# Kernel tuning notes

Hardware: AMD Instinct MI355X
Metric: run time of the kernel (lower is better)

## Reference

```python
import jax, jax.numpy as jnp
import numpy as np

D_MODEL = 1024
N_HEADS = 16
D_HEAD = D_MODEL // N_HEADS
D_FF = 4096
B, S = 4, 1024
EPS = 1e-12


def layer_norm(x, gamma, beta):
    # Faithful to the torch module: unbiased std (ddof=1) and division by (std + eps).
    mean = jnp.mean(x, axis=-1, keepdims=True)
    var = jnp.sum((x - mean) ** 2, axis=-1, keepdims=True) / (x.shape[-1] - 1)
    std = jnp.sqrt(var)
    return gamma * (x - mean) / (std + EPS) + beta


def setup_inputs() -> dict:
    key = jax.random.key(0)
    ks = jax.random.split(key, 10)
    sc = lambda fan_in: 1.0 / np.sqrt(fan_in)
    inp = {
        "x": jax.random.normal(ks[0], (B, S, D_MODEL), dtype=jnp.float32),
        "ln1_g": jnp.ones((D_MODEL,), jnp.float32),
        "ln1_b": jnp.zeros((D_MODEL,), jnp.float32),
        "wq": jax.random.normal(ks[1], (D_MODEL, D_MODEL), jnp.float32) * sc(D_MODEL),
        "bq": jnp.zeros((D_MODEL,), jnp.float32),
        "wk": jax.random.normal(ks[2], (D_MODEL, D_MODEL), jnp.float32) * sc(D_MODEL),
        "bk": jnp.zeros((D_MODEL,), jnp.float32),
        "wv": jax.random.normal(ks[3], (D_MODEL, D_MODEL), jnp.float32) * sc(D_MODEL),
        "bv": jnp.zeros((D_MODEL,), jnp.float32),
        "ln2_g": jnp.ones((D_MODEL,), jnp.float32),
        "ln2_b": jnp.zeros((D_MODEL,), jnp.float32),
        "w1": jax.random.normal(ks[4], (D_FF, D_MODEL), jnp.float32) * sc(D_MODEL),
        "b1": jnp.zeros((D_FF,), jnp.float32),
        "w2": jax.random.normal(ks[5], (D_MODEL, D_FF), jnp.float32) * sc(D_FF),
        "b2": jnp.zeros((D_MODEL,), jnp.float32),
    }
    return inp


def reference(x, ln1_g, ln1_b, wq, bq, wk, bk, wv, bv, ln2_g, ln2_b, w1, b1, w2, b2):
    Bsz, Sq, D = x.shape
    residual = x
    h = layer_norm(x, ln1_g, ln1_b)
    # QKV projections (no output projection in the original module)
    q = (h @ wq.T + bq).reshape(Bsz, Sq, N_HEADS, D_HEAD)
    k = (h @ wk.T + bk).reshape(Bsz, Sq, N_HEADS, D_HEAD)
    v = (h @ wv.T + bv).reshape(Bsz, Sq, N_HEADS, D_HEAD)
    scores = jnp.einsum("bqhd,bkhd->bhqk", q, k) / np.sqrt(D_HEAD)
    attn = jax.nn.softmax(scores, axis=-1)  # [B, H, S, S]
    ctx = jnp.einsum("bhqk,bkhd->bqhd", attn, v).reshape(Bsz, Sq, D)
    out = ctx + residual
    residual = out
    h2 = layer_norm(out, ln2_g, ln2_b)
    # 1x1 conv FFN == per-token MLP with ReLU (dropout inactive at eval)
    ff = jax.nn.relu(h2 @ w1.T + b1) @ w2.T + b2
    out = ff + residual
    # torch returns attn flattened head-major: [H*B, S, S]
    attn_ret = jnp.transpose(attn, (1, 0, 2, 3)).reshape(N_HEADS * Bsz, Sq, Sq)
    return out, attn_ret
```

## Files before the change

### kernel.cpp

```cpp
#include <hip/hip_runtime.h>
#include <cstdint>
#include <cstddef>

#define SEQ 1024
#define DM 1024
#define DF 4096
#define NH 16
#define DH 64
#define BSZ 4
#define NTOK (BSZ*SEQ)
#define QKVSZ ((long)NTOK*DM)

typedef short s16x8 __attribute__((ext_vector_type(8)));
typedef float f32x4 __attribute__((ext_vector_type(4)));

__device__ __forceinline__ unsigned short f2bf(float f) {
  union { float f; unsigned u; } c; c.f = f;
  unsigned u = c.u;
  return (unsigned short)((u + 0x7fffu + ((u >> 16) & 1u)) >> 16);
}
__device__ __forceinline__ float bf2f(unsigned short b) {
  union { unsigned u; float f; } c; c.u = ((unsigned)b) << 16; return c.f;
}

__device__ __forceinline__ void gll16(const void* g, void* l) {
  __builtin_amdgcn_global_load_lds(
      (__attribute__((address_space(1))) void*)(g),
      (__attribute__((address_space(3))) void*)(l), 16, 0, 0);
}

template<int BM, int BN, int WM, int WN, int EPI>
__launch_bounds__(256)
__global__ void gemm_k(const unsigned short* __restrict__ A,
                       const unsigned short* __restrict__ W,
                       const float* __restrict__ bias,
                       void* __restrict__ outp,
                       const float* __restrict__ resid,
                       int nB, int K, int aRow, int wRow, int oRow,
                       float scale) {
  constexpr int BK = 32;
  __shared__ unsigned short At[BM*BK];
  __shared__ unsigned short Wt[BN*BK];
  const int tid = threadIdx.x;
  const int kz = blockIdx.y;
  A += (long)kz * K;
  W += (long)kz * K;
  float* outF = (float*)outp;
  if (EPI == 7) outF += (long)kz * ((long)(gridDim.x / nB) * BM) * oRow;
  const int mb = (int)blockIdx.x / nB, nb = (int)blockIdx.x % nB;
  const long aBase = (long)mb*BM*aRow;
  const long wBase = (long)nb*BN*wRow;
  const int wave = tid >> 6, lane = tid & 63;
  const int quad = lane >> 4, l16 = lane & 15;
  constexpr int WGN = BN / WN;
  const int wm = (wave / WGN) * WM, wn = (wave % WGN) * WN;
  constexpr int MT = WM/16, NT = WN/16;
  f32x4 acc[MT][NT] = {};
  const int srow = tid >> 2, skof = (tid & 3) * 8;

  for (int k0 = 0; k0 < K; k0 += BK) {
#pragma unroll
    for (int r = 0; r < BM; r += 64)
      gll16(A + aBase + (long)(r + srow)*aRow + k0 + skof, &At[(r + srow)*BK + skof]);
#pragma unroll
    for (int r = 0; r < BN; r += 64)
      gll16(W + wBase + (long)(r + srow)*wRow + k0 + skof, &Wt[(r + srow)*BK + skof]);
    __syncthreads();
    s16x8 af[MT];
#pragma unroll
    for (int mt = 0; mt < MT; ++mt)
      af[mt] = *(const s16x8*)&At[(wm + mt*16 + l16)*BK + quad*8];
#pragma unroll
    for (int nt = 0; nt < NT; ++nt) {
      s16x8 bfr = *(const s16x8*)&Wt[(wn + nt*16 + l16)*BK + quad*8];
#pragma unroll
      for (int mt = 0; mt < MT; ++mt)
        acc[mt][nt] = __builtin_amdgcn_mfma_f32_16x16x32_bf16(af[mt], bfr, acc[mt][nt], 0, 0, 0);
    }
    __syncthreads();
  }

#pragma unroll
  for (int mt = 0; mt < MT; ++mt) {
#pragma unroll
    for (int nt = 0; nt < NT; ++nt) {
      const int gn = nb*BN + wn + nt*16 + l16;
      const float bv = bias ? bias[gn] : 0.f;
      if (EPI == 5) {
        unsigned short* base = (unsigned short*)outp;
        const int reg = gn >> 10, cn = gn & 1023;
        if (reg == 2) {
          const int gm0 = mb*BM + wm + mt*16 + quad*4;
          const int bb = gm0 >> 10, s0 = gm0 & 1023;
          ushort4 o4;
          o4.x = f2bf(acc[mt][nt][0] + bv);
          o4.y = f2bf(acc[mt][nt][1] + bv);
          o4.z = f2bf(acc[mt][nt][2] + bv);
          o4.w = f2bf(acc[mt][nt][3] + bv);
          *(ushort4*)&base[2*QKVSZ + (long)bb*DM*SEQ + (long)cn*SEQ + s0] = o4;
        } else {
#pragma unroll
          for (int r = 0; r < 4; ++r) {
            const int gm = mb*BM + wm + mt*16 + quad*4 + r;
            const float v = acc[mt][nt][r] + bv;
            if (reg == 0) base[(long)gm*DM + cn] = f2bf(v * scale);
            else          base[QKVSZ + (long)gm*DM + cn] = f2bf(v);
          }
        }
      } else {
#pragma unroll
        for (int r = 0; r < 4; ++r) {
          const int gm = mb*BM + wm + mt*16 + quad*4 + r;
          float v = acc[mt][nt][r] + bv;
          if (EPI == 1) {
            ((unsigned short*)outp)[(long)gm*oRow + gn] = f2bf(v > 0.f ? v : 0.f);
          } else if (EPI == 3) {
            const long o = (long)gm*oRow + gn;
            ((float*)outp)[o] = v + resid[o];
          } else if (EPI == 7) {
            outF[(long)gm*oRow + gn] = v;
          }
        }
      }
    }
  }
}

__launch_bounds__(256)
__global__ void comb_k(const float* __restrict__ p,
                       const float* __restrict__ b2,
                       const float* __restrict__ out1,
                       float* __restrict__ out) {
  const int i = blockIdx.x * 256 + threadIdx.x;
  const float4 a = ((const float4*)p)[i];
  const float4 b = ((const float4*)(p + (long)NTOK*DM))[i];
  const float4 bb = ((const float4*)b2)[i & (DM/4 - 1)];
  const float4 r = ((const float4*)out1)[i];
  float4 o;
  o.x = a.x + b.x + bb.x + r.x;
  o.y = a.y + b.y + bb.y + r.y;
  o.z = a.z + b.z + bb.z + r.z;
  o.w = a.w + b.w + bb.w + r.w;
  ((float4*)out)[i] = o;
}

__launch_bounds__(256)
__global__ void ln_k(const float* __restrict__ x, const float* __restrict__ g,
                     const float* __restrict__ bta, unsigned short* __restrict__ out) {
  const int row = blockIdx.x, t = threadIdx.x;
  const float4 v = ((const float4*)(x + (long)row*DM))[t];
  __shared__ float red[4];
  float s = v.x + v.y + v.z + v.w;
#pragma unroll
  for (int o = 32; o; o >>= 1) s += __shfl_down(s, o);
  if ((t & 63) == 0) red[t >> 6] = s;
  __syncthreads();
  const float mean = (red[0] + red[1] + red[2] + red[3]) * (1.f/1024.f);
  __syncthreads();
  const float dx = v.x - mean, dy = v.y - mean, dz = v.z - mean, dw = v.w - mean;
  float sq = dx*dx + dy*dy + dz*dz + dw*dw;
#pragma unroll
  for (int o = 32; o; o >>= 1) sq += __shfl_down(sq, o);
  if ((t & 63) == 0) red[t >> 6] = sq;
  __syncthreads();
  const float var = (red[0] + red[1] + red[2] + red[3]) * (1.f/1023.f);
  const float inv = 1.f / (sqrtf(var) + 1e-12f);
  const float4 gv = ((const float4*)g)[t];
  const float4 bv = ((const float4*)bta)[t];
  ushort4 o4;
  o4.x = f2bf(gv.x * dx * inv + bv.x);
  o4.y = f2bf(gv.y * dy * inv + bv.y);
  o4.z = f2bf(gv.z * dz * inv + bv.z);
  o4.w = f2bf(gv.w * dw * inv + bv.w);
  ((ushort4*)(out + (long)row*DM))[t] = o4;
}

#define R_WQ  262144L
#define R_WK  524288L
#define R_WV  786432L
#define R_W1  1835008L
#define R_W2  2883584L
#define CVT_BLOCKS 11265
__launch_bounds__(256)
__global__ void cvt5_k(const float* __restrict__ wq, const float* __restrict__ wk,
                       const float* __restrict__ wv, const float* __restrict__ w1,
                       const float* __restrict__ w2,
                       const float* __restrict__ bq, const float* __restrict__ bk,
                       const float* __restrict__ bvv,
                       unsigned short* __restrict__ wqkvb,
                       unsigned short* __restrict__ w1b,
                       unsigned short* __restrict__ w2b,
                       float* __restrict__ bcat) {
  const long blk = blockIdx.x;
  if (blk == CVT_BLOCKS - 1) {
    for (int j = threadIdx.x; j < 3072; j += 256)
      bcat[j] = j < 1024 ? bq[j] : (j < 2048 ? bk[j - 1024] : bvv[j - 2048]);
    return;
  }
  long i = blk*256 + threadIdx.x;
  const float* s; unsigned short* d;
  if (i < R_WQ)       { s = wq; d = wqkvb;              }
  else if (i < R_WK)  { s = wk; d = wqkvb + 1048576; i -= R_WQ; }
  else if (i < R_WV)  { s = wv; d = wqkvb + 2097152; i -= R_WK; }
  else if (i < R_W1)  { s = w1; d = w1b;             i -= R_WV; }
  else                { s = w2; d = w2b;             i -= R_W1; }
  const float4 v = ((const float4*)s)[i];
  ushort4 o; o.x = f2bf(v.x); o.y = f2bf(v.y); o.z = f2bf(v.z); o.w = f2bf(v.w);
  ((ushort4*)d)[i] = o;
}

#define LDP 1032
__launch_bounds__(256)
__global__ void attn_k(const unsigned short* __restrict__ Q,
                       const unsigned short* __restrict__ Kb,
                       const unsigned short* __restrict__ vt,
                       const float* __restrict__ xres,
                       float* __restrict__ attn_f,
                       float* __restrict__ out1) {
  const int b = blockIdx.y, h = blockIdx.z;
  const int q0 = blockIdx.x * 16;
  const int wave = threadIdx.x >> 6, lane = threadIdx.x & 63;
  const int quad = lane >> 4, l16 = lane & 15;
  __shared__ unsigned short PL[16 * LDP];
  __shared__ float red[4][16];

  const unsigned short* Qb = Q + (long)b*SEQ*DM + h*DH;
  const unsigned short* Kh = Kb + (long)b*SEQ*DM + h*DH;
  s16x8 af[2];
#pragma unroll
  for (int ks = 0; ks < 2; ++ks)
    af[ks] = *(const s16x8*)&Qb[(long)(q0 + l16)*DM + ks*32 + quad*8];
  f32x4 acc[16];
#pragma unroll
  for (int nt = 0; nt < 16; ++nt) acc[nt] = (f32x4){0.f, 0.f, 0.f, 0.f};
  for (int nt = 0; nt < 16; ++nt) {
    const int kc = wave*256 + nt*16 + l16;
#pragma unroll
    for (int ks = 0; ks < 2; ++ks) {
      const s16x8 bfr = *(const s16x8*)&Kh[(long)kc*DM + ks*32 + quad*8];
      acc[nt] = __builtin_amdgcn_mfma_f32_16x16x32_bf16(af[ks], bfr, acc[nt], 0, 0, 0);
    }
  }

  float rmax[4];
#pragma unroll
  for (int r = 0; r < 4; ++r) {
    float m = -3e38f;
#pragma unroll
    for (int nt = 0; nt < 16; ++nt) m = fmaxf(m, acc[nt][r]);
#pragma unroll
    for (int o = 1; o < 16; o <<= 1) m = fmaxf(m, __shfl_xor(m, o));
    rmax[r] = m;
  }
  if (l16 == 0) {
#pragma unroll
    for (int r = 0; r < 4; ++r) red[wave][quad*4 + r] = rmax[r];
  }
  __syncthreads();
#pragma unroll
  for (int r = 0; r < 4; ++r)
    rmax[r] = fmaxf(fmaxf(red[0][quad*4+r], red[1][quad*4+r]),
                    fmaxf(red[2][quad*4+r], red[3][quad*4+r]));
  __syncthreads();
#pragma unroll
  for (int r = 0; r < 4; ++r) {
    float s = 0.f;
#pragma unroll
    for (int nt = 0; nt < 16; ++nt) {
      const float e = __expf(acc[nt][r] - rmax[r]);
      acc[nt][r] = e; s += e;
    }
#pragma unroll
    for (int o = 1; o < 16; o <<= 1) s += __shfl_xor(s, o);
    if (l16 == 0) red[wave][quad*4 + r] = s;
  }
  __syncthreads();

  const long obase = (long)(h*BSZ + b)*SEQ*SEQ + (long)q0*SEQ;
#pragma unroll
  for (int r = 0; r < 4; ++r) {
    const float tot = red[0][quad*4+r] + red[1][quad*4+r] + red[2][quad*4+r] + red[3][quad*4+r];
    const float inv = 1.f / tot;
    unsigned short* prow = &PL[(quad*4 + r)*LDP + wave*256 + l16];
    float* arow = attn_f + obase + (long)(quad*4 + r)*SEQ + wave*256 + l16;
#pragma unroll
    for (int nt = 0; nt < 16; ++nt) {
      const float pv_ = acc[nt][r] * inv;
      prow[nt*16] = f2bf(pv_);
      arow[nt*16] = pv_;
    }
  }
  __syncthreads();

  f32x4 cc[4] = {};
  const unsigned short* Vh = vt + (long)b*DM*SEQ + (long)(h*DH + wave*16 + l16)*SEQ;
#pragma unroll
  for (int k0 = 0; k0 < 32; ++k0) {
    const s16x8 a  = *(const s16x8*)&PL[l16*LDP + k0*32 + quad*8];
    const s16x8 bf = *(const s16x8*)&Vh[k0*32 + quad*8];
    cc[k0 & 3] = __builtin_amdgcn_mfma_f32_16x16x32_bf16(a, bf, cc[k0 & 3], 0, 0, 0);
  }
  const f32x4 c = (cc[0] + cc[1]) + (cc[2] + cc[3]);

#pragma unroll
  for (int r = 0; r < 4; ++r) {
    const int gq = q0 + quad*4 + r;
    const int col = h*DH + wave*16 + l16;
    const long idx = (long)b*SEQ*DM + (long)gq*DM + col;
    out1[idx] = c[r] + xres[idx];
  }
}

extern "C" void kernel_launch(void* const* d_in, const int* in_sizes, int n_in,
                              void* d_out, int out_size, void* d_ws, size_t ws_size,
                              hipStream_t stream) {
  const float* x    = (const float*)d_in[0];
  const float* ln1g = (const float*)d_in[1];
  const float* ln1b = (const float*)d_in[2];
  const float* wq   = (const float*)d_in[3];
  const float* bq   = (const float*)d_in[4];
  const float* wk   = (const float*)d_in[5];
  const float* bk   = (const float*)d_in[6];
  const float* wv   = (const float*)d_in[7];
  const float* bv   = (const float*)d_in[8];
  const float* ln2g = (const float*)d_in[9];
  const float* ln2b = (const float*)d_in[10];
  const float* w1   = (const float*)d_in[11];
  const float* b1   = (const float*)d_in[12];
  const float* w2   = (const float*)d_in[13];
  const float* b2   = (const float*)d_in[14];
  float* out    = (float*)d_out;
  float* attn_f = out + (long)NTOK*DM;

  uint8_t* p = (uint8_t*)d_ws;
  auto alloc = [&](size_t bytes) {
    uint8_t* r = p; p += (bytes + 255) & ~(size_t)255; return r;
  };
  unsigned short* hbuf  = (unsigned short*)alloc((size_t)NTOK*DM*2);
  unsigned short* qkv   = (unsigned short*)alloc((size_t)3*NTOK*DM*2);
  unsigned short* h2    = (unsigned short*)alloc((size_t)NTOK*DM*2);
  unsigned short* f1    = (unsigned short*)alloc((size_t)NTOK*DF*2);
  float*          out1  = (float*)alloc((size_t)NTOK*DM*4);
  unsigned short* wqkvb = (unsigned short*)alloc((size_t)3*DM*DM*2);
  unsigned short* w1b   = (unsigned short*)alloc((size_t)DF*DM*2);
  unsigned short* w2b   = (unsigned short*)alloc((size_t)DM*DF*2);
  float*          bcat  = (float*)alloc((size_t)3*DM*4);
  float*          part  = (float*)alloc((size_t)2*NTOK*DM*4);

  cvt5_k<<<CVT_BLOCKS, 256, 0, stream>>>(wq, wk, wv, w1, w2, bq, bk, bv,
                                         wqkvb, w1b, w2b, bcat);
  ln_k<<<NTOK, 256, 0, stream>>>(x, ln1g, ln1b, hbuf);

  gemm_k<128,128,64,64,5><<<dim3((NTOK/128)*(3*DM/128)), 256, 0, stream>>>(
      hbuf, wqkvb, bcat, qkv, nullptr, 3*DM/128, DM, DM, DM, DM, 0.125f);

  attn_k<<<dim3(SEQ/16, BSZ, NH), 256, 0, stream>>>(
      qkv, qkv + QKVSZ, qkv + 2*QKVSZ, x, attn_f, out1);

  ln_k<<<NTOK, 256, 0, stream>>>(out1, ln2g, ln2b, h2);

  gemm_k<128,128,64,64,1><<<dim3((NTOK/128)*(DF/128)), 256, 0, stream>>>(
      h2, w1b, b1, f1, nullptr, DF/128, DM, DM, DM, DF, 1.f);

  gemm_k<128,128,64,64,7><<<dim3((NTOK/128)*(DM/128), 2), 256, 0, stream>>>(
      f1, w2b, nullptr, part, nullptr, DM/128, DF/2, DF, DF, DM, 1.f);
  comb_k<<<(NTOK*DM)/1024, 256, 0, stream>>>(part, b2, out1, out);
}
```

Baseline: 649.4 us.

## Replace GEMM with 256x256 double-buffered 8-wave kernel and 4-way split-K

Replaces the simple 128x128 BK=32 GEMM with a 256x256 tile, BK=64, 8-wave kernel. It double-buffers LDS through direct global-to-LDS loads with an XOR swizzle, interleaves staging into four MFMA phases with barriers and s_setprio, and remaps workgroups for XCD locality. The FFN2 GEMM moves to 4-way split-K, and the combine kernel now sums four partial planes. This targets load latency and LDS bank conflicts and raises per-tile reuse, at the cost of 128KB of LDS per block, fewer blocks, and more partial-sum traffic.

```diff
diff --git a/kernel.cpp b/kernel.cpp
--- a/kernel.cpp
+++ b/kernel.cpp
@@ -29,68 +29,108 @@
       (__attribute__((address_space(3))) void*)(l), 16, 0, 0);
 }
 
-template<int BM, int BN, int WM, int WN, int EPI>
-__launch_bounds__(256)
-__global__ void gemm_k(const unsigned short* __restrict__ A,
-                       const unsigned short* __restrict__ W,
-                       const float* __restrict__ bias,
-                       void* __restrict__ outp,
-                       const float* __restrict__ resid,
-                       int nB, int K, int aRow, int wRow, int oRow,
-                       float scale) {
-  constexpr int BK = 32;
-  __shared__ unsigned short At[BM*BK];
-  __shared__ unsigned short Wt[BN*BK];
+template<int EPI>
+__launch_bounds__(512, 2)
+__global__ void gemm8_k(const unsigned short* __restrict__ A,
+                        const unsigned short* __restrict__ W,
+                        const float* __restrict__ bias,
+                        void* __restrict__ outp,
+                        int nNB, int K, int aRow, int wRow, int oRow,
+                        float scale, long planeStride) {
+  __shared__ __align__(16) char smem[131072];
   const int tid = threadIdx.x;
   const int kz = blockIdx.y;
-  A += (long)kz * K;
-  W += (long)kz * K;
-  float* outF = (float*)outp;
-  if (EPI == 7) outF += (long)kz * ((long)(gridDim.x / nB) * BM) * oRow;
-  const int mb = (int)blockIdx.x / nB, nb = (int)blockIdx.x % nB;
-  const long aBase = (long)mb*BM*aRow;
-  const long wBase = (long)nb*BN*wRow;
+  const int cpx = (int)gridDim.x >> 3;
+  const int wgid = ((int)blockIdx.x & 7) * cpx + ((int)blockIdx.x >> 3);
+  const int mb = wgid / nNB, nb = wgid % nNB;
+  const unsigned short* Ag = A + (long)mb*256*aRow + (long)kz*K;
+  const unsigned short* Wg = W + (long)nb*256*wRow + (long)kz*K;
   const int wave = tid >> 6, lane = tid & 63;
   const int quad = lane >> 4, l16 = lane & 15;
-  constexpr int WGN = BN / WN;
-  const int wm = (wave / WGN) * WM, wn = (wave % WGN) * WN;
-  constexpr int MT = WM/16, NT = WN/16;
-  f32x4 acc[MT][NT] = {};
-  const int srow = tid >> 2, skof = (tid & 3) * 8;
-
-  for (int k0 = 0; k0 < K; k0 += BK) {
-#pragma unroll
-    for (int r = 0; r < BM; r += 64)
-      gll16(A + aBase + (long)(r + srow)*aRow + k0 + skof, &At[(r + srow)*BK + skof]);
-#pragma unroll
-    for (int r = 0; r < BN; r += 64)
-      gll16(W + wBase + (long)(r + srow)*wRow + k0 + skof, &Wt[(r + srow)*BK + skof]);
-    __syncthreads();
-    s16x8 af[MT];
-#pragma unroll
-    for (int mt = 0; mt < MT; ++mt)
-      af[mt] = *(const s16x8*)&At[(wm + mt*16 + l16)*BK + quad*8];
-#pragma unroll
-    for (int nt = 0; nt < NT; ++nt) {
-      s16x8 bfr = *(const s16x8*)&Wt[(wn + nt*16 + l16)*BK + quad*8];
-#pragma unroll
-      for (int mt = 0; mt < MT; ++mt)
-        acc[mt][nt] = __builtin_amdgcn_mfma_f32_16x16x32_bf16(af[mt], bfr, acc[mt][nt], 0, 0, 0);
+  const int wr = wave >> 2, wc = wave & 3;
+  const int srow = tid >> 3, sch = tid & 7;
+  const int swz = sch ^ (srow & 7);
+  const int ldst = tid << 4;
+  f32x4 acc[8][4] = {};
+
+  auto stageA = [&](int q, int t, int buf) {
+    gll16(Ag + (long)(q*64 + srow)*aRow + t*64 + swz*8,
+          smem + buf*32768 + q*8192 + ldst);
+  };
+  auto stageB = [&](int q, int t, int buf) {
+    gll16(Wg + (long)(q*64 + srow)*wRow + t*64 + swz*8,
+          smem + 65536 + buf*32768 + q*8192 + ldst);
+  };
+
+  const int NTt = K >> 6;
+  stageA(0,0,0); stageA(2,0,0); stageA(1,0,0); stageA(3,0,0);
+  stageB(0,0,0); stageB(1,0,0); stageB(2,0,0); stageB(3,0,0);
+  if (NTt > 1) {
+    stageA(0,1,1); stageA(2,1,1);
+    asm volatile("s_waitcnt vmcnt(2)" ::: "memory");
+  } else {
+    asm volatile("s_waitcnt vmcnt(0)" ::: "memory");
+  }
+  asm volatile("" ::: "memory"); __builtin_amdgcn_s_barrier();
+  asm volatile("" ::: "memory");
+
+  for (int t = 0; t < NTt; ++t) {
+    const int cur = t & 1, nxt = cur ^ 1;
+    const char* Ab = smem + cur*32768;
+    const char* Bb = smem + 65536 + cur*32768;
+
+#define G8_PHASE(MHF, NHF, STAGE_STMT, WAIT_STMT)                                \
+    {                                                                            \
+      s16x8 afr[4][2]; s16x8 bfr[2][2];                                          \
+      _Pragma("unroll") for (int mf = 0; mf < 4; ++mf)                           \
+      _Pragma("unroll") for (int ks = 0; ks < 2; ++ks) {                         \
+        const int ra = wr*128 + MHF*64 + mf*16 + l16;                            \
+        afr[mf][ks] = *(const s16x8*)(Ab + ra*128 + (((ks*4+quad)^(ra&7))<<4));  \
+      }                                                                          \
+      _Pragma("unroll") for (int nf = 0; nf < 2; ++nf)                           \
+      _Pragma("unroll") for (int ks = 0; ks < 2; ++ks) {                         \
+        const int rb = wc*64 + NHF*32 + nf*16 + l16;                             \
+        bfr[nf][ks] = *(const s16x8*)(Bb + rb*128 + (((ks*4+quad)^(rb&7))<<4));  \
+      }                                                                          \
+      STAGE_STMT;                                                                \
+      WAIT_STMT;                                                                 \
+      asm volatile("" ::: "memory"); __builtin_amdgcn_s_barrier();               \
+      asm volatile("" ::: "memory");                                             \
+      __builtin_amdgcn_s_setprio(1);                                             \
+      _Pragma("unroll") for (int nf = 0; nf < 2; ++nf)                           \
+      _Pragma("unroll") for (int mf = 0; mf < 4; ++mf)                           \
+      _Pragma("unroll") for (int ks = 0; ks < 2; ++ks)                           \
+        acc[MHF*4+mf][NHF*2+nf] = __builtin_amdgcn_mfma_f32_16x16x32_bf16(       \
+            afr[mf][ks], bfr[nf][ks], acc[MHF*4+mf][NHF*2+nf], 0, 0, 0);         \
+      __builtin_amdgcn_s_setprio(0);                                             \
+      asm volatile("" ::: "memory"); __builtin_amdgcn_s_barrier();               \
+      asm volatile("" ::: "memory");                                             \
     }
-    __syncthreads();
-  }
-
-#pragma unroll
-  for (int mt = 0; mt < MT; ++mt) {
-#pragma unroll
-    for (int nt = 0; nt < NT; ++nt) {
-      const int gn = nb*BN + wn + nt*16 + l16;
-      const float bv = bias ? bias[gn] : 0.f;
+
+    G8_PHASE(0, 0,
+      if (t+1 < NTt) { stageA(1, t+1, nxt); stageA(3, t+1, nxt); }, )
+    G8_PHASE(0, 1,
+      if (t+1 < NTt) { stageB(0, t+1, nxt); stageB(1, t+1, nxt); }, )
+    G8_PHASE(1, 0,
+      if (t+1 < NTt) { stageB(2, t+1, nxt); stageB(3, t+1, nxt); }, )
+    G8_PHASE(1, 1,
+      if (t+2 < NTt) { stageA(0, t+2, cur); stageA(2, t+2, cur); },
+      if (t+2 < NTt) { asm volatile("s_waitcnt vmcnt(2)" ::: "memory"); }
+      else if (t+1 < NTt) { asm volatile("s_waitcnt vmcnt(0)" ::: "memory"); })
+#undef G8_PHASE
+  }
+
+#pragma unroll
+  for (int mt = 0; mt < 8; ++mt) {
+#pragma unroll
+    for (int nt = 0; nt < 4; ++nt) {
+      const int gn = nb*256 + wc*64 + nt*16 + l16;
+      const float bv = (EPI == 1 || EPI == 5) ? bias[gn] : 0.f;
       if (EPI == 5) {
         unsigned short* base = (unsigned short*)outp;
         const int reg = gn >> 10, cn = gn & 1023;
         if (reg == 2) {
-          const int gm0 = mb*BM + wm + mt*16 + quad*4;
+          const int gm0 = mb*256 + wr*128 + mt*16 + quad*4;
           const int bb = gm0 >> 10, s0 = gm0 & 1023;
           ushort4 o4;
           o4.x = f2bf(acc[mt][nt][0] + bv);
@@ -101,7 +141,7 @@
         } else {
 #pragma unroll
           for (int r = 0; r < 4; ++r) {
-            const int gm = mb*BM + wm + mt*16 + quad*4 + r;
+            const int gm = mb*256 + wr*128 + mt*16 + quad*4 + r;
             const float v = acc[mt][nt][r] + bv;
             if (reg == 0) base[(long)gm*DM + cn] = f2bf(v * scale);
             else          base[QKVSZ + (long)gm*DM + cn] = f2bf(v);
@@ -110,15 +150,12 @@
       } else {
 #pragma unroll
         for (int r = 0; r < 4; ++r) {
-          const int gm = mb*BM + wm + mt*16 + quad*4 + r;
-          float v = acc[mt][nt][r] + bv;
+          const int gm = mb*256 + wr*128 + mt*16 + quad*4 + r;
+          const float v = acc[mt][nt][r] + bv;
           if (EPI == 1) {
             ((unsigned short*)outp)[(long)gm*oRow + gn] = f2bf(v > 0.f ? v : 0.f);
-          } else if (EPI == 3) {
-            const long o = (long)gm*oRow + gn;
-            ((float*)outp)[o] = v + resid[o];
           } else if (EPI == 7) {
-            outF[(long)gm*oRow + gn] = v;
+            ((float*)outp)[(long)kz*planeStride + (long)gm*oRow + gn] = v;
           }
         }
       }
@@ -132,15 +169,17 @@
                        const float* __restrict__ out1,
                        float* __restrict__ out) {
   const int i = blockIdx.x * 256 + threadIdx.x;
-  const float4 a = ((const float4*)p)[i];
-  const float4 b = ((const float4*)(p + (long)NTOK*DM))[i];
+  const float4 a0 = ((const float4*)p)[i];
+  const float4 a1 = ((const float4*)(p + (long)NTOK*DM))[i];
+  const float4 a2 = ((const float4*)(p + 2L*NTOK*DM))[i];
+  const float4 a3 = ((const float4*)(p + 3L*NTOK*DM))[i];
   const float4 bb = ((const float4*)b2)[i & (DM/4 - 1)];
   const float4 r = ((const float4*)out1)[i];
   float4 o;
-  o.x = a.x + b.x + bb.x + r.x;
-  o.y = a.y + b.y + bb.y + r.y;
-  o.z = a.z + b.z + bb.z + r.z;
-  o.w = a.w + b.w + bb.w + r.w;
+  o.x = (a0.x + a1.x) + (a2.x + a3.x) + bb.x + r.x;
+  o.y = (a0.y + a1.y) + (a2.y + a3.y) + bb.y + r.y;
+  o.z = (a0.z + a1.z) + (a2.z + a3.z) + bb.z + r.z;
+  o.w = (a0.w + a1.w) + (a2.w + a3.w) + bb.w + r.w;
   ((float4*)out)[i] = o;
 }
 
@@ -345,24 +384,24 @@
   unsigned short* w1b   = (unsigned short*)alloc((size_t)DF*DM*2);
   unsigned short* w2b   = (unsigned short*)alloc((size_t)DM*DF*2);
   float*          bcat  = (float*)alloc((size_t)3*DM*4);
-  float*          part  = (float*)alloc((size_t)2*NTOK*DM*4);
+  float*          part  = (float*)alloc((size_t)4*NTOK*DM*4);
 
   cvt5_k<<<CVT_BLOCKS, 256, 0, stream>>>(wq, wk, wv, w1, w2, bq, bk, bv,
                                          wqkvb, w1b, w2b, bcat);
   ln_k<<<NTOK, 256, 0, stream>>>(x, ln1g, ln1b, hbuf);
 
-  gemm_k<128,128,64,64,5><<<dim3((NTOK/128)*(3*DM/128)), 256, 0, stream>>>(
-      hbuf, wqkvb, bcat, qkv, nullptr, 3*DM/128, DM, DM, DM, DM, 0.125f);
+  gemm8_k<5><<<dim3((NTOK/256)*(3*DM/256)), 512, 0, stream>>>(
+      hbuf, wqkvb, bcat, qkv, 3*DM/256, DM, DM, DM, DM, 0.125f, 0);
 
   attn_k<<<dim3(SEQ/16, BSZ, NH), 256, 0, stream>>>(
       qkv, qkv + QKVSZ, qkv + 2*QKVSZ, x, attn_f, out1);
 
   ln_k<<<NTOK, 256, 0, stream>>>(out1, ln2g, ln2b, h2);
 
-  gemm_k<128,128,64,64,1><<<dim3((NTOK/128)*(DF/128)), 256, 0, stream>>>(
-      h2, w1b, b1, f1, nullptr, DF/128, DM, DM, DM, DF, 1.f);
-
-  gemm_k<128,128,64,64,7><<<dim3((NTOK/128)*(DM/128), 2), 256, 0, stream>>>(
-      f1, w2b, nullptr, part, nullptr, DM/128, DF/2, DF, DF, DM, 1.f);
+  gemm8_k<1><<<dim3((NTOK/256)*(DF/256)), 512, 0, stream>>>(
+      h2, w1b, b1, f1, DF/256, DM, DM, DM, DF, 1.f, 0);
+
+  gemm8_k<7><<<dim3((NTOK/256)*(DM/256), 4), 512, 0, stream>>>(
+      f1, w2b, nullptr, part, DM/256, DF/4, DF, DF, DM, 1.f, (long)NTOK*DM);
   comb_k<<<(NTOK*DM)/1024, 256, 0, stream>>>(part, b2, out1, out);
 }
```

After: 611.6 us. 5.8% less time.
